# Performance work log

Measured on AMD Instinct MI355X. Metric: run time of the kernel, lower is better.

## Reference

```python
import jax, jax.numpy as jnp
import numpy as np

N, E, F_IN, HID, L_EXTRA, G = 50000, 800000, 128, 128, 3, 256

def gcn_conv(x, W, b, src, dst, norm):
    # PyG GCNConv: out = D^-1/2 (A+I) D^-1/2 (X W) + b  (self-loops included in src/dst)
    xw = x @ W                                  # [N, out]
    msg = xw[src] * norm[:, None]               # [E+N, out]
    return jax.ops.segment_sum(msg, dst, num_segments=N) + b

def setup_inputs() -> dict:
    key = jax.random.key(0)
    ks = jax.random.split(key, 12)
    x = jax.random.normal(ks[0], (N, F_IN), dtype=jnp.float32)
    edge_index = jax.random.randint(ks[1], (2, E), 0, N, dtype=jnp.int64)
    batch = jnp.sort(jax.random.randint(ks[2], (N,), 0, G, dtype=jnp.int64))
    s = 1.0 / np.sqrt(HID)
    W0 = jax.random.uniform(ks[3], (F_IN, HID), jnp.float32, -s, s)
    b0 = jnp.zeros((HID,), jnp.float32)
    Wh = jax.random.uniform(ks[4], (L_EXTRA, HID, HID), jnp.float32, -s, s)
    bh = jnp.zeros((L_EXTRA, HID), jnp.float32)
    s1 = 1.0 / np.sqrt(3 * HID)
    lin1_w = jax.random.uniform(ks[5], (3 * HID, HID), jnp.float32, -s1, s1)
    lin1_b = jax.random.uniform(ks[6], (HID,), jnp.float32, -s1, s1)
    s2 = 1.0 / np.sqrt(HID)
    lin2_w = jax.random.uniform(ks[7], (HID, 2), jnp.float32, -s2, s2)
    lin2_b = jax.random.uniform(ks[8], (2,), jnp.float32, -s2, s2)
    return {"x": x, "edge_index": edge_index, "batch": batch,
            "W0": W0, "b0": b0, "Wh": Wh, "bh": bh,
            "lin1_w": lin1_w, "lin1_b": lin1_b, "lin2_w": lin2_w, "lin2_b": lin2_b}

def reference(x, edge_index, batch, W0, b0, Wh, bh, lin1_w, lin1_b, lin2_w, lin2_b):
    # add self-loops once (shared by all layers)
    loop = jnp.arange(N, dtype=edge_index.dtype)
    src = jnp.concatenate([edge_index[0], loop])
    dst = jnp.concatenate([edge_index[1], loop])
    deg = jax.ops.segment_sum(jnp.ones_like(dst, dtype=x.dtype), dst, num_segments=N)
    dinv = jnp.where(deg > 0, jax.lax.rsqrt(deg), 0.0)
    norm = dinv[src] * dinv[dst]                # [E+N]

    h = jax.nn.relu(gcn_conv(x, W0, b0, src, dst, norm))
    for i in range(L_EXTRA):
        h = jax.nn.relu(gcn_conv(h, Wh[i], bh[i], src, dst, norm))

    # multi-pool over graphs in the batch
    p_sum = jax.ops.segment_sum(h, batch, num_segments=G)
    cnt = jax.ops.segment_sum(jnp.ones((N,), h.dtype), batch, num_segments=G)
    p_mean = p_sum / jnp.maximum(cnt, 1.0)[:, None]
    p_max = jax.ops.segment_max(h, batch, num_segments=G)
    p_max = jnp.where(jnp.isfinite(p_max), p_max, 0.0)  # guard empty graphs
    g = jnp.concatenate([p_sum, p_mean, p_max], axis=1)  # [G, 3*HID]

    g = jax.nn.relu(g @ lin1_w + lin1_b)        # dropout p=0.5 is identity in eval
    logits = g @ lin2_w + lin2_b
    return jax.nn.log_softmax(logits, axis=-1)
```

## Files before the change

### kernel.cpp

```cpp
#include <hip/hip_runtime.h>
#include <hip/hip_fp16.h>
#include <cstddef>

typedef _Float16 f16x8 __attribute__((ext_vector_type(8)));
typedef float f32x4 __attribute__((ext_vector_type(4)));
typedef unsigned short ushort8 __attribute__((ext_vector_type(8)));


__global__ __launch_bounds__(256) void k_bhist(const int* __restrict__ dst, int* __restrict__ bcnt, int e) {
    __shared__ int lh[256];
    int t = threadIdx.x;
    lh[t] = 0;
    __syncthreads();
    for (int i = blockIdx.x * 256 + t; i < e; i += gridDim.x * 256)
        atomicAdd(&lh[dst[i] >> 8], 1);
    __syncthreads();
    if (lh[t] > 0) atomicAdd(&bcnt[t], lh[t]);
}

__global__ __launch_bounds__(256) void k_bscan(const int* __restrict__ bcnt, int* __restrict__ bebase,
                                               int* __restrict__ bcbase, int* __restrict__ bcur,
                                               int* __restrict__ rowptr, int nbk, int n, int e) {
    __shared__ int se[256], sc[256];
    int t = threadIdx.x;
    int ec = (t < nbk) ? bcnt[t] : 0;
    int nodes = 0;
    if (t < nbk) {
        nodes = n - t * 256;
        if (nodes > 256) nodes = 256;
        if (nodes < 0) nodes = 0;
    }
    se[t] = ec;
    sc[t] = ec + nodes;
    __syncthreads();
    for (int off = 1; off < 256; off <<= 1) {
        int ve = (t >= off) ? se[t - off] : 0;
        int vc = (t >= off) ? sc[t - off] : 0;
        __syncthreads();
        se[t] += ve;
        sc[t] += vc;
        __syncthreads();
    }
    if (t < nbk) {
        bebase[t] = se[t] - ec;
        bcbase[t] = sc[t] - (ec + nodes);
        bcur[t]   = se[t] - ec;
    }
    if (t == 0) {
        bebase[nbk] = e;
        rowptr[n] = e + n;
    }
}

__global__ __launch_bounds__(256) void k_bscatter(const int* __restrict__ src, const int* __restrict__ dst,
                                                  int* __restrict__ bcur, int2* __restrict__ bedges, int e) {
    __shared__ int lh[256];
    __shared__ int gbase[256];
    int t = threadIdx.x;
    lh[t] = 0;
    __syncthreads();
    int base = blockIdx.x * 4096;
    int s_[16], d_[16];
#pragma unroll
    for (int u = 0; u < 16; ++u) {
        int j = base + u * 256 + t;
        if (j < e) {
            s_[u] = src[j];
            d_[u] = dst[j];
            atomicAdd(&lh[d_[u] >> 8], 1);
        } else {
            d_[u] = -1;
        }
    }
    __syncthreads();
    if (lh[t] > 0) gbase[t] = atomicAdd(&bcur[t], lh[t]);
    __syncthreads();
    lh[t] = 0;
    __syncthreads();
#pragma unroll
    for (int u = 0; u < 16; ++u) {
        if (d_[u] >= 0) {
            int bk = d_[u] >> 8;
            int lpos = atomicAdd(&lh[bk], 1);
            bedges[gbase[bk] + lpos] = make_int2(s_[u], d_[u]);
        }
    }
}

__global__ __launch_bounds__(256) void k_bcsr(const int2* __restrict__ bedges, const int* __restrict__ bebase,
                                              const int* __restrict__ bcbase, int* __restrict__ rowptr,
                                              float* __restrict__ dinv, int* __restrict__ csr_s, int n) {
    __shared__ int lh[256], lcur[256];
    int b = blockIdx.x, t = threadIdx.x;
    int n0 = b << 8;
    int nb = n - n0; if (nb > 256) nb = 256;
    int e0 = bebase[b], e1 = bebase[b + 1];
    int cb = bcbase[b];
    lh[t] = 0;
    __syncthreads();
    for (int i = e0 + t; i < e1; i += 256)
        atomicAdd(&lh[bedges[i].y - n0], 1);
    __syncthreads();
    int deg = (t < nb) ? (lh[t] + 1) : 0;
    __syncthreads();
    lh[t] = deg;
    __syncthreads();
    for (int off = 1; off < 256; off <<= 1) {
        int v = (t >= off) ? lh[t - off] : 0;
        __syncthreads();
        lh[t] += v;
        __syncthreads();
    }
    int lrp = lh[t] - deg;
    if (t < nb) {
        rowptr[n0 + t] = cb + lrp;
        dinv[n0 + t] = rsqrtf((float)deg);
    }
    lcur[t] = lrp;
    __syncthreads();
    for (int i = e0 + t; i < e1; i += 256) {
        int2 ed = bedges[i];
        int pos = cb + atomicAdd(&lcur[ed.y - n0], 1);
        csr_s[pos] = ed.x;
    }
    if (t < nb) {
        int pos = cb + atomicAdd(&lcur[t], 1);
        csr_s[pos] = n0 + t;
    }
}

__global__ __launch_bounds__(256) void k_wprep(const float* __restrict__ W0, const float* __restrict__ Wh,
                                               __half* __restrict__ WP, int* __restrict__ bcnt, int nlayers) {
    int layer = blockIdx.x;
    int t = threadIdx.x;
    if (layer >= nlayers) {
        bcnt[t] = 0;
        return;
    }
    const float* W = (layer == 0) ? W0 : Wh + (size_t)(layer - 1) * 16384;
    __half* out = WP + (size_t)layer * 16384;
    for (int u = 0; u < 64; ++u) {
        int o = u * 256 + t;
        int i  = o & 7;
        int l  = (o >> 3) & 63;
        int kc = (o >> 9) & 3;
        int nt = o >> 11;
        int k   = kc * 32 + ((l >> 4) << 3) + i;
        int col = nt * 16 + (l & 15);
        out[o] = __float2half(W[k * 128 + col]);
    }
}

__global__ __launch_bounds__(256) void k_gemm(const __half* __restrict__ H, const __half* __restrict__ WP,
                                              const float* __restrict__ dinv, __half* __restrict__ O,
                                              int n) {
    __shared__ __half wl[16384];
    const int t = threadIdx.x;
#pragma unroll
    for (int u = 0; u < 8; ++u) {
        int idx = (u * 256 + t) * 8;
        *(ushort8*)&wl[idx] = *(const ushort8*)&WP[idx];
    }
    const int wid = t >> 6, l = t & 63;
    const int row0 = blockIdx.x * 128 + wid * 32;
    const int ar = l & 15, g = l >> 4;

    f16x8 a[2][4];
    float dv[2][4];
#pragma unroll
    for (int mt = 0; mt < 2; ++mt) {
        int row = row0 + mt * 16 + ar;
        int rc = min(row, n - 1);
#pragma unroll
        for (int kc = 0; kc < 4; ++kc)
            a[mt][kc] = *(const f16x8*)&H[(size_t)rc * 128 + kc * 32 + g * 8];
#pragma unroll
        for (int r = 0; r < 4; ++r) {
            int orow = row0 + mt * 16 + g * 4 + r;
            dv[mt][r] = dinv[min(orow, n - 1)];
        }
    }
    __syncthreads();

#pragma unroll
    for (int nt = 0; nt < 8; ++nt) {
        f16x8 b[4];
#pragma unroll
        for (int kc = 0; kc < 4; ++kc)
            b[kc] = *(f16x8*)&wl[((nt * 4 + kc) * 64 + l) * 8];
#pragma unroll
        for (int mt = 0; mt < 2; ++mt) {
            f32x4 acc = {0.f, 0.f, 0.f, 0.f};
#pragma unroll
            for (int kc = 0; kc < 4; ++kc)
                acc = __builtin_amdgcn_mfma_f32_16x16x32_f16(a[mt][kc], b[kc], acc, 0, 0, 0);
#pragma unroll
            for (int r = 0; r < 4; ++r) {
                int orow = row0 + mt * 16 + g * 4 + r;
                if (orow < n)
                    O[(size_t)orow * 128 + nt * 16 + ar] = __float2half(acc[r] * dv[mt][r]);
            }
        }
    }
}

__global__ __launch_bounds__(256) void k_gemm32(const float* __restrict__ H, const __half* __restrict__ WP,
                                                const float* __restrict__ dinv, __half* __restrict__ O,
                                                int n) {
    __shared__ __half wl[16384];
    const int t = threadIdx.x;
#pragma unroll
    for (int u = 0; u < 8; ++u) {
        int idx = (u * 256 + t) * 8;
        *(ushort8*)&wl[idx] = *(const ushort8*)&WP[idx];
    }
    const int wid = t >> 6, l = t & 63;
    const int row0 = blockIdx.x * 128 + wid * 32;
    const int ar = l & 15, g = l >> 4;

    f16x8 a[2][4];
    float dv[2][4];
#pragma unroll
    for (int mt = 0; mt < 2; ++mt) {
        int row = row0 + mt * 16 + ar;
        int rc = min(row, n - 1);
#pragma unroll
        for (int kc = 0; kc < 4; ++kc) {
            float4 p0 = *(const float4*)&H[(size_t)rc * 128 + kc * 32 + g * 8];
            float4 p1 = *(const float4*)&H[(size_t)rc * 128 + kc * 32 + g * 8 + 4];
            f16x8 av;
            av[0] = (_Float16)p0.x; av[1] = (_Float16)p0.y; av[2] = (_Float16)p0.z; av[3] = (_Float16)p0.w;
            av[4] = (_Float16)p1.x; av[5] = (_Float16)p1.y; av[6] = (_Float16)p1.z; av[7] = (_Float16)p1.w;
            a[mt][kc] = av;
        }
#pragma unroll
        for (int r = 0; r < 4; ++r) {
            int orow = row0 + mt * 16 + g * 4 + r;
            dv[mt][r] = dinv[min(orow, n - 1)];
        }
    }
    __syncthreads();

#pragma unroll
    for (int nt = 0; nt < 8; ++nt) {
        f16x8 b[4];
#pragma unroll
        for (int kc = 0; kc < 4; ++kc)
            b[kc] = *(f16x8*)&wl[((nt * 4 + kc) * 64 + l) * 8];
#pragma unroll
        for (int mt = 0; mt < 2; ++mt) {
            f32x4 acc = {0.f, 0.f, 0.f, 0.f};
#pragma unroll
            for (int kc = 0; kc < 4; ++kc)
                acc = __builtin_amdgcn_mfma_f32_16x16x32_f16(a[mt][kc], b[kc], acc, 0, 0, 0);
#pragma unroll
            for (int r = 0; r < 4; ++r) {
                int orow = row0 + mt * 16 + g * 4 + r;
                if (orow < n)
                    O[(size_t)orow * 128 + nt * 16 + ar] = __float2half(acc[r] * dv[mt][r]);
            }
        }
    }
}

__global__ __launch_bounds__(256) void k_agg(const __half* __restrict__ XW, const int* __restrict__ cs,
                                             const int* __restrict__ rp, const float* __restrict__ dinv,
                                             const float* __restrict__ bias, __half* __restrict__ Hn, int n) {
    int wid  = (blockIdx.x * 256 + threadIdx.x) >> 6;
    int lane = threadIdx.x & 63;
    if (wid >= n) return;
    int s = rp[wid], e = rp[wid + 1];
    const __half2* X2 = (const __half2*)XW;
    float ax[8], ay[8];
#pragma unroll
    for (int u = 0; u < 8; ++u) { ax[u] = 0.f; ay[u] = 0.f; }
    for (int base = s; base < e; base += 64) {
        int m = e - base;
        if (m > 64) m = 64;
        int myi = (lane < m) ? cs[base + lane] : 0;
        int j = 0;
        for (; j + 8 <= m; j += 8) {
            int idx[8];
#pragma unroll
            for (int u = 0; u < 8; ++u) idx[u] = __shfl(myi, j + u);
            float2 v[8];
#pragma unroll
            for (int u = 0; u < 8; ++u) v[u] = __half22float2(X2[(size_t)idx[u] * 64 + lane]);
#pragma unroll
            for (int u = 0; u < 8; ++u) { ax[u] += v[u].x; ay[u] += v[u].y; }
        }
        for (; j < m; ++j) {
            int i0 = __shfl(myi, j);
            float2 v = __half22float2(X2[(size_t)i0 * 64 + lane]);
            ax[j & 7] += v.x;
            ay[j & 7] += v.y;
        }
    }
    float a0 = (ax[0] + ax[1]) + (ax[2] + ax[3]) + ((ax[4] + ax[5]) + (ax[6] + ax[7]));
    float a1 = (ay[0] + ay[1]) + (ay[2] + ay[3]) + ((ay[4] + ay[5]) + (ay[6] + ay[7]));
    float dvv = dinv[wid];
    int f = lane * 2;
    a0 = fmaxf(fmaf(a0, dvv, bias[f]),     0.f);
    a1 = fmaxf(fmaf(a1, dvv, bias[f + 1]), 0.f);
    ((__half2*)Hn)[(size_t)wid * 64 + lane] = __floats2half2_rn(a0, a1);
}

__global__ __launch_bounds__(256) void k_poolhead(const __half* __restrict__ H, const int* __restrict__ batch,
                                                  const float* __restrict__ w1, const float* __restrict__ b1,
                                                  const float* __restrict__ w2, const float* __restrict__ b2,
                                                  float* __restrict__ out, int n) {
    __shared__ float lsum[16][128];
    __shared__ float lmax[16][128];
    __shared__ float gv[384];
    __shared__ float o1[128];
    __shared__ int bnd[2];
    int g = blockIdx.x, t = threadIdx.x;
    if (t < 2) {
        int key = g + t;
        int lo = 0, hi = n;
        while (lo < hi) {
            int mid = (lo + hi) >> 1;
            if (batch[mid] < key) lo = mid + 1; else hi = mid;
        }
        bnd[t] = lo;
    }
    __syncthreads();
    const int s = bnd[0], e = bnd[1];
    const int rg = t >> 4, fb = t & 15;
    float sum8[8], max8[8];
#pragma unroll
    for (int j = 0; j < 8; ++j) { sum8[j] = 0.f; max8[j] = 0.f; }
    for (int r = s + rg; r < e; r += 16) {
        f16x8 v = *(const f16x8*)&H[(size_t)r * 128 + fb * 8];
#pragma unroll
        for (int j = 0; j < 8; ++j) {
            float x = (float)v[j];
            sum8[j] += x;
            max8[j] = fmaxf(max8[j], x);
        }
    }
#pragma unroll
    for (int j = 0; j < 8; ++j) {
        lsum[rg][fb * 8 + j] = sum8[j];
        lmax[rg][fb * 8 + j] = max8[j];
    }
    __syncthreads();
    if (t < 128) {
        float sum = 0.f, mx = 0.f;
#pragma unroll
        for (int r = 0; r < 16; ++r) {
            sum += lsum[r][t];
            mx = fmaxf(mx, lmax[r][t]);
        }
        float cnt = (float)(e - s);
        gv[t]       = sum;
        gv[128 + t] = sum / fmaxf(cnt, 1.f);
        gv[256 + t] = mx;
    }
    __syncthreads();
    if (t < 128) {
        float acc = b1[t];
#pragma unroll 8
        for (int k = 0; k < 384; ++k) acc = fmaf(gv[k], w1[k * 128 + t], acc);
        o1[t] = fmaxf(acc, 0.f);
    }
    __syncthreads();
    if (t < 64) {
        float p0 = o1[t] * w2[t * 2 + 0] + o1[t + 64] * w2[(t + 64) * 2 + 0];
        float p1 = o1[t] * w2[t * 2 + 1] + o1[t + 64] * w2[(t + 64) * 2 + 1];
        for (int off = 32; off > 0; off >>= 1) {
            p0 += __shfl_down(p0, off);
            p1 += __shfl_down(p1, off);
        }
        if (t == 0) {
            float l0 = p0 + b2[0], l1 = p1 + b2[1];
            float m = fmaxf(l0, l1);
            float lse = m + logf(expf(l0 - m) + expf(l1 - m));
            out[g * 2 + 0] = l0 - lse;
            out[g * 2 + 1] = l1 - lse;
        }
    }
}


extern "C" void kernel_launch(void* const* d_in, const int* in_sizes, int n_in,
                              void* d_out, int out_size, void* d_ws, size_t ws_size,
                              hipStream_t stream) {
    const float* x     = (const float*)d_in[0];
    const int*   ei    = (const int*)d_in[1];
    const int*   batch = (const int*)d_in[2];
    const float* W0    = (const float*)d_in[3];
    const float* b0    = (const float*)d_in[4];
    const float* Wh    = (const float*)d_in[5];
    const float* bh    = (const float*)d_in[6];
    const float* l1w   = (const float*)d_in[7];
    const float* l1b   = (const float*)d_in[8];
    const float* l2w   = (const float*)d_in[9];
    const float* l2b   = (const float*)d_in[10];
    float* out = (float*)d_out;

    const int N  = in_sizes[0] / 128;
    const int E  = in_sizes[1] / 2;
    const int G  = out_size / 2;
    const int LX = in_sizes[5] / (128 * 128);
    const int NB = (N + 255) / 256;

    const int* src = ei;
    const int* dst = ei + E;

    char* p = (char*)d_ws;
    auto alloc = [&](size_t bytes) -> void* {
        void* r = (void*)p;
        p += (bytes + 255) & ~(size_t)255;
        return r;
    };
    int*    rowptr = (int*)alloc((size_t)(N + 1) * 4);
    float*  dinv   = (float*)alloc((size_t)N * 4);
    int*    bcnt   = (int*)alloc(1040);
    int*    bebase = (int*)alloc(1040);
    int*    bcbase = (int*)alloc(1040);
    int*    bcur   = (int*)alloc(1040);
    int*    csr_s  = (int*)alloc((size_t)(E + N) * 4);
    int2*   bedges = (int2*)alloc((size_t)E * 8);
    __half* h16    = (__half*)alloc((size_t)N * 128 * 2);
    __half* xw16   = (__half*)alloc((size_t)N * 128 * 2);
    __half* wp     = (__half*)alloc((size_t)(LX + 1) * 16384 * 2);

    k_wprep<<<LX + 2, 256, 0, stream>>>(W0, Wh, wp, bcnt, LX + 1);

    k_bhist<<<NB, 256, 0, stream>>>(dst, bcnt, E);
    k_bscan<<<1, 256, 0, stream>>>(bcnt, bebase, bcbase, bcur, rowptr, NB, N, E);
    k_bscatter<<<(E + 4095) / 4096, 256, 0, stream>>>(src, dst, bcur, bedges, E);
    k_bcsr<<<NB, 256, 0, stream>>>(bedges, bebase, bcbase, rowptr, dinv, csr_s, N);

    const int gemmBlocks = (N + 127) / 128;
    const int aggBlocks  = (N + 3) / 4;

    k_gemm32<<<gemmBlocks, 256, 0, stream>>>(x, wp, dinv, xw16, N);
    k_agg<<<aggBlocks, 256, 0, stream>>>(xw16, csr_s, rowptr, dinv, b0, h16, N);
    for (int l = 0; l < LX; ++l) {
        k_gemm<<<gemmBlocks, 256, 0, stream>>>(h16, wp + (size_t)(l + 1) * 16384, dinv, xw16, N);
        k_agg<<<aggBlocks, 256, 0, stream>>>(xw16, csr_s, rowptr, dinv, bh + (size_t)l * 128, h16, N);
    }

    k_poolhead<<<G, 256, 0, stream>>>(h16, batch, l1w, l1b, l2w, l2b, out, N);
}
```

Baseline: 263.3 us.

## Pack bucketed edges into one int and gather rows with 16-byte loads

The bucketed edge list now stores src<<8 | local dst in a single int instead of an int2, which halves the scatter and CSR-build traffic. The aggregation kernel is restructured so that each wave processes 4 edges at a time. Each of 16 lanes loads 8 halves (16 bytes) per row, and partial sums are combined with cross-lane xor shuffles before one lane group writes the output. The risk is the shuffle reduction overhead and idle lanes on low-degree nodes, and the packing requires src < 2^23, which holds for N=50000.

```diff
diff --git a/kernel.cpp b/kernel.cpp
--- a/kernel.cpp
+++ b/kernel.cpp
@@ -53,7 +53,7 @@
 }
 
 __global__ __launch_bounds__(256) void k_bscatter(const int* __restrict__ src, const int* __restrict__ dst,
-                                                  int* __restrict__ bcur, int2* __restrict__ bedges, int e) {
+                                                  int* __restrict__ bcur, int* __restrict__ bedges, int e) {
     __shared__ int lh[256];
     __shared__ int gbase[256];
     int t = threadIdx.x;
@@ -82,12 +82,12 @@
         if (d_[u] >= 0) {
             int bk = d_[u] >> 8;
             int lpos = atomicAdd(&lh[bk], 1);
-            bedges[gbase[bk] + lpos] = make_int2(s_[u], d_[u]);
-        }
-    }
-}
-
-__global__ __launch_bounds__(256) void k_bcsr(const int2* __restrict__ bedges, const int* __restrict__ bebase,
+            bedges[gbase[bk] + lpos] = (s_[u] << 8) | (d_[u] & 255);
+        }
+    }
+}
+
+__global__ __launch_bounds__(256) void k_bcsr(const int* __restrict__ bedges, const int* __restrict__ bebase,
                                               const int* __restrict__ bcbase, int* __restrict__ rowptr,
                                               float* __restrict__ dinv, int* __restrict__ csr_s, int n) {
     __shared__ int lh[256], lcur[256];
@@ -99,7 +99,7 @@
     lh[t] = 0;
     __syncthreads();
     for (int i = e0 + t; i < e1; i += 256)
-        atomicAdd(&lh[bedges[i].y - n0], 1);
+        atomicAdd(&lh[bedges[i] & 255], 1);
     __syncthreads();
     int deg = (t < nb) ? (lh[t] + 1) : 0;
     __syncthreads();
@@ -119,9 +119,9 @@
     lcur[t] = lrp;
     __syncthreads();
     for (int i = e0 + t; i < e1; i += 256) {
-        int2 ed = bedges[i];
-        int pos = cb + atomicAdd(&lcur[ed.y - n0], 1);
-        csr_s[pos] = ed.x;
+        int ed = bedges[i];
+        int pos = cb + atomicAdd(&lcur[ed & 255], 1);
+        csr_s[pos] = (int)((unsigned)ed >> 8);
     }
     if (t < nb) {
         int pos = cb + atomicAdd(&lcur[t], 1);
@@ -270,39 +270,47 @@
     int lane = threadIdx.x & 63;
     if (wid >= n) return;
     int s = rp[wid], e = rp[wid + 1];
-    const __half2* X2 = (const __half2*)XW;
-    float ax[8], ay[8];
-#pragma unroll
-    for (int u = 0; u < 8; ++u) { ax[u] = 0.f; ay[u] = 0.f; }
+    const int g = lane >> 4, fs = lane & 15;
+    float acc0[8], acc1[8];
+#pragma unroll
+    for (int k = 0; k < 8; ++k) { acc0[k] = 0.f; acc1[k] = 0.f; }
     for (int base = s; base < e; base += 64) {
         int m = e - base;
         if (m > 64) m = 64;
         int myi = (lane < m) ? cs[base + lane] : 0;
-        int j = 0;
-        for (; j + 8 <= m; j += 8) {
-            int idx[8];
-#pragma unroll
-            for (int u = 0; u < 8; ++u) idx[u] = __shfl(myi, j + u);
-            float2 v[8];
-#pragma unroll
-            for (int u = 0; u < 8; ++u) v[u] = __half22float2(X2[(size_t)idx[u] * 64 + lane]);
-#pragma unroll
-            for (int u = 0; u < 8; ++u) { ax[u] += v[u].x; ay[u] += v[u].y; }
-        }
-        for (; j < m; ++j) {
-            int i0 = __shfl(myi, j);
-            float2 v = __half22float2(X2[(size_t)i0 * 64 + lane]);
-            ax[j & 7] += v.x;
-            ay[j & 7] += v.y;
-        }
-    }
-    float a0 = (ax[0] + ax[1]) + (ax[2] + ax[3]) + ((ax[4] + ax[5]) + (ax[6] + ax[7]));
-    float a1 = (ay[0] + ay[1]) + (ay[2] + ay[3]) + ((ay[4] + ay[5]) + (ay[6] + ay[7]));
-    float dvv = dinv[wid];
-    int f = lane * 2;
-    a0 = fmaxf(fmaf(a0, dvv, bias[f]),     0.f);
-    a1 = fmaxf(fmaf(a1, dvv, bias[f + 1]), 0.f);
-    ((__half2*)Hn)[(size_t)wid * 64 + lane] = __floats2half2_rn(a0, a1);
+#pragma unroll 2
+        for (int j = 0; j < m; j += 8) {
+            int ia = __shfl(myi, j + g);
+            int ib = __shfl(myi, j + 4 + g);
+            if (j + g < m) {
+                f16x8 va = *(const f16x8*)&XW[(size_t)ia * 128 + fs * 8];
+#pragma unroll
+                for (int k = 0; k < 8; ++k) acc0[k] += (float)va[k];
+            }
+            if (j + 4 + g < m) {
+                f16x8 vb = *(const f16x8*)&XW[(size_t)ib * 128 + fs * 8];
+#pragma unroll
+                for (int k = 0; k < 8; ++k) acc1[k] += (float)vb[k];
+            }
+        }
+    }
+#pragma unroll
+    for (int k = 0; k < 8; ++k) acc0[k] += acc1[k];
+#pragma unroll
+    for (int k = 0; k < 8; ++k) acc0[k] += __shfl_xor(acc0[k], 16);
+#pragma unroll
+    for (int k = 0; k < 8; ++k) acc0[k] += __shfl_xor(acc0[k], 32);
+    if (g == 0) {
+        float dvv = dinv[wid];
+        float4 bb0 = *(const float4*)&bias[fs * 8];
+        float4 bb1 = *(const float4*)&bias[fs * 8 + 4];
+        float bb[8] = {bb0.x, bb0.y, bb0.z, bb0.w, bb1.x, bb1.y, bb1.z, bb1.w};
+        f16x8 o;
+#pragma unroll
+        for (int k = 0; k < 8; ++k)
+            o[k] = (_Float16)fmaxf(fmaf(acc0[k], dvv, bb[k]), 0.f);
+        *(f16x8*)&Hn[(size_t)wid * 128 + fs * 8] = o;
+    }
 }
 
 __global__ __launch_bounds__(256) void k_poolhead(const __half* __restrict__ H, const int* __restrict__ batch,
@@ -421,7 +429,7 @@
     int*    bcbase = (int*)alloc(1040);
     int*    bcur   = (int*)alloc(1040);
     int*    csr_s  = (int*)alloc((size_t)(E + N) * 4);
-    int2*   bedges = (int2*)alloc((size_t)E * 8);
+    int*    bedges = (int*)alloc((size_t)E * 4);
     __half* h16    = (__half*)alloc((size_t)N * 128 * 2);
     __half* xw16   = (__half*)alloc((size_t)N * 128 * 2);
     __half* wp     = (__half*)alloc((size_t)(LX + 1) * 16384 * 2);
```

Result: faster. 249.5 us (-5.2%).
